# Kernel tuning notes

Hardware: AMD Instinct MI355X
Metric: run time of the kernel (lower is better)

The kernel has to match this reference:

```python
import jax, jax.numpy as jnp
import numpy as np

C, NC, B, T, H, W = 64, 4, 4, 8, 96, 96
BT = B * T
_DN = ('NCDHW', 'OIDHW', 'NCDHW')


def setup_inputs() -> dict:
    key = jax.random.key(0)
    ks = jax.random.split(key, 16)
    r = lambda i, shape, s=0.02: jax.random.normal(ks[i], shape, jnp.float32) * s
    f32 = jnp.float32
    return {
        'x': jax.random.normal(ks[0], (BT, C, H, W), f32),
        't': T,
        'temporal_kernels': r(1, (NC, C)),            # (num_components, C) per-channel kernel scale
        'kernel_weights': jnp.ones((NC,), f32),
        'length_scales': jnp.ones((NC,), f32),
        'temporal_basis': r(2, (C, T)),               # (C, 8) learned temporal basis
        'sc_w1': r(3, (C // 8, C), 0.05), 'sc_b1': jnp.zeros((C // 8,), f32),
        'sc_w2': r(4, (2 * C, C // 8), 0.05), 'sc_b2': jnp.zeros((2 * C,), f32),
        'diff_w': r(5, (C, 1, 3, 1, 1), 0.1),         # depthwise temporal conv
        'diff_gamma': jnp.ones((C,), f32), 'diff_beta': jnp.zeros((C,), f32),
        'diff_mean': r(6, (C,), 0.1),
        'diff_var': jnp.ones((C,), f32) + 0.1 * jax.random.uniform(ks[7], (C,), f32),
        'unc_w1': r(8, (C // 4, C), 0.05), 'unc_b1': jnp.zeros((C // 4,), f32),
        'unc_w2': r(9, (2, C // 4), 0.05), 'unc_b2': jnp.zeros((2,), f32),
        'pool_w': r(10, (C, C, 3, 1, 1), 0.02), 'pool_b': jnp.zeros((C,), f32),
        'proj_w': r(11, (C, C), 0.05),                # spectral-normalized 1x1x1 conv
        'bn_gamma': jnp.ones((C,), f32), 'bn_beta': jnp.zeros((C,), f32),
        'bn_mean': r(12, (C,), 0.1),
        'bn_var': jnp.ones((C,), f32) + 0.1 * jax.random.uniform(ks[13], (C,), f32),
        'temperature': jnp.float32(1.0),
    }


def _bc(v):
    return v[None, :, None, None, None]


def reference(x, t, temporal_kernels, kernel_weights, length_scales, temporal_basis,
              sc_w1, sc_b1, sc_w2, sc_b2,
              diff_w, diff_gamma, diff_beta, diff_mean, diff_var,
              unc_w1, unc_b1, unc_w2, unc_b2,
              pool_w, pool_b, proj_w,
              bn_gamma, bn_beta, bn_mean, bn_var, temperature):
    bt, c, h, w = x.shape
    b = bt // t
    x5 = x.reshape(b, t, c, h, w).transpose(0, 2, 1, 3, 4)   # (b,c,t,h,w)

    # --- Gaussian process temporal attention: per-channel (t,t) RBF mixture kernel ---
    ti = jnp.arange(t, dtype=x.dtype)
    dt2 = (ti[:, None] - ti[None, :]) ** 2                    # (t,t)
    ls = jnp.exp(length_scales)                               # (nc,)
    rbf = jnp.exp(-dt2[None] / (2.0 * ls[:, None, None] ** 2))  # (nc,t,t)
    wts = jax.nn.softmax(kernel_weights)
    K = jnp.einsum('i,ic,ist->cst', wts, temporal_kernels, rbf)  # (c,t,t)
    gp = jnp.einsum('cst,bctn->bcsn', K, x5.reshape(b, c, t, h * w)).reshape(b, c, t, h, w)

    # --- stochastic temporal sampling (eval: deterministic importance mask) ---
    mask = jax.nn.softmax(temporal_basis.mean(axis=0))        # (t,)
    stoch = x5 * mask[None, None, :, None, None]

    # --- spatial covariance gate (global pooled MLP -> sigmoid gate) ---
    g = x5.mean(axis=(2, 3, 4))                               # (b,c)
    h1 = jax.nn.gelu(g @ sc_w1.T + sc_b1, approximate=False)
    cov = h1 @ sc_w2.T + sc_b2                                # (b,2c); second half = cov_var
    cov_w = jax.nn.sigmoid(cov[:, c:])[:, :, None, None, None]
    fused0 = gp * cov_w + stoch * (1.0 - cov_w)

    # --- diffusion: depthwise temporal conv + BN(eval) + GELU ---
    d = jax.lax.conv_general_dilated(fused0, diff_w, (1, 1, 1), ((1, 1), (0, 0), (0, 0)),
                                     dimension_numbers=_DN, feature_group_count=c)
    d = _bc(diff_gamma) * (d - _bc(diff_mean)) / jnp.sqrt(_bc(diff_var) + 1e-5) + _bc(diff_beta)
    d = jax.nn.gelu(d, approximate=False)

    # --- uncertainty head + precision-weighted fusion ---
    u = jax.nn.gelu(jnp.einsum('bcthw,oc->bothw', d, unc_w1) + _bc(unc_b1), approximate=False)
    u = jnp.einsum('bcthw,oc->bothw', u, unc_w2) + _bc(unc_b2)  # (b,2,t,h,w)
    mu, var = u[:, :1], u[:, 1:]
    prec = 1.0 / (var + 1e-6)
    fused = (mu * prec + d) / (prec + 1.0)

    # --- temporal pool: temporal conv then global spatial mean ---
    p = jax.lax.conv_general_dilated(fused, pool_w, (1, 1, 1), ((1, 1), (0, 0), (0, 0)),
                                     dimension_numbers=_DN) + _bc(pool_b)
    out = fused + p.mean(axis=(3, 4), keepdims=True)

    # --- spectral-normalized 1x1x1 projection + BN(eval) ---
    sigma = jnp.linalg.svd(proj_w, compute_uv=False)[0]
    out = jnp.einsum('bcthw,oc->bothw', out, proj_w / sigma)
    out = _bc(bn_gamma) * (out - _bc(bn_mean)) / jnp.sqrt(_bc(bn_var) + 1e-5) + _bc(bn_beta)

    out = out.transpose(0, 2, 1, 3, 4).reshape(bt, c, h, w)
    return x + jnp.tanh(temperature) * out
```

## Files before the change

kernel.cpp:

```cpp
#include <hip/hip_runtime.h>
#include <math.h>

#define C64 64
#define NCK 4
#define BB  4
#define TT  8
#define HH  96
#define WW  96
#define HW  9216
#define CHW (C64*HW)
#define NTILE 32
#define NBLK_PER_B (HW/NTILE)

#define OFF_GSUM 0
#define OFF_S    256
#define OFF_COVW 2304
#define OFF_K    2560
#define OFF_MASK 6656
#define OFF_AC   6664
#define OFF_BC   6728
#define OFF_P2   6792
#define OFF_B2   10888
#define OFF_BIAS3 10952
#define ZERO_N   2304

__device__ __forceinline__ float gelu_f(float v) {
    return 0.5f * v * (1.0f + erff(v * 0.70710678118654752f));
}
__device__ __forceinline__ unsigned short f2bf(float f) {
    union { float f; unsigned int u; } v; v.f = f;
    unsigned int r = (v.u + 0x7fffu + ((v.u >> 16) & 1u)) >> 16;
    return (unsigned short)r;
}
__device__ __forceinline__ float bf2f(unsigned short h) {
    union { unsigned int u; float f; } v; v.u = ((unsigned int)h) << 16;
    return v.f;
}

__global__ __launch_bounds__(256) void k1_gsum(const float* __restrict__ x,
                                               float* __restrict__ ws) {
    const int blk = blockIdx.x;
    const float4* p = reinterpret_cast<const float4*>(x + (size_t)blk * HW);
    float s = 0.f;
    for (int i = threadIdx.x; i < HW / 4; i += 256) {
        float4 v = p[i];
        s += v.x + v.y + v.z + v.w;
    }
    #pragma unroll
    for (int off = 32; off; off >>= 1) s += __shfl_down(s, off, 64);
    __shared__ float part[4];
    const int wid = threadIdx.x >> 6, lane = threadIdx.x & 63;
    if (lane == 0) part[wid] = s;
    __syncthreads();
    if (threadIdx.x == 0) {
        float t = part[0] + part[1] + part[2] + part[3];
        int c = blk % C64;
        int b = (blk / C64) / TT;
        atomicAdd(ws + OFF_GSUM + b * C64 + c, t);
    }
}

__global__ __launch_bounds__(256) void k2_prep(
    const float* __restrict__ tk, const float* __restrict__ kw,
    const float* __restrict__ lsc, const float* __restrict__ tb,
    const float* __restrict__ sc_w1, const float* __restrict__ sc_b1,
    const float* __restrict__ sc_w2, const float* __restrict__ sc_b2,
    const float* __restrict__ diff_gamma, const float* __restrict__ diff_beta,
    const float* __restrict__ diff_mean, const float* __restrict__ diff_var,
    const float* __restrict__ proj_w,
    const float* __restrict__ bn_gamma, const float* __restrict__ bn_beta,
    const float* __restrict__ bn_mean, const float* __restrict__ bn_var,
    const float* __restrict__ temperature,
    float* __restrict__ ws) {
    __shared__ float gsh[BB * C64];
    __shared__ float h1[BB][8];
    __shared__ float wtss[NCK], lss[NCK];
    __shared__ float Msh[64 * 64];
    __shared__ float M2sh[64 * 64];
    __shared__ float v0[64], v1[64];
    __shared__ float lamsh;
    const int tid = threadIdx.x;

    gsh[tid] = ws[OFF_GSUM + tid] * (1.0f / ((float)TT * (float)HW));
    __syncthreads();

    if (tid < BB * 8) {
        int b = tid >> 3, j = tid & 7;
        float a = sc_b1[j];
        for (int c = 0; c < C64; c++) a += gsh[b * C64 + c] * sc_w1[j * C64 + c];
        h1[b][j] = gelu_f(a);
    }
    if (tid == 0) {
        float mx = -1e30f;
        for (int i = 0; i < NCK; i++) mx = fmaxf(mx, kw[i]);
        float e[NCK], s = 0.f;
        for (int i = 0; i < NCK; i++) { e[i] = expf(kw[i] - mx); s += e[i]; }
        for (int i = 0; i < NCK; i++) { wtss[i] = e[i] / s; lss[i] = expf(lsc[i]); }
    }
    if (tid == 1) {
        float m[TT], mx = -1e30f;
        for (int t = 0; t < TT; t++) {
            float a = 0.f;
            for (int c = 0; c < C64; c++) a += tb[c * TT + t];
            m[t] = a * (1.0f / (float)C64);
            mx = fmaxf(mx, m[t]);
        }
        float s = 0.f;
        for (int t = 0; t < TT; t++) { m[t] = expf(m[t] - mx); s += m[t]; }
        for (int t = 0; t < TT; t++) ws[OFF_MASK + t] = m[t] / s;
    }
    __syncthreads();

    {
        int b = tid >> 6, c = tid & 63;
        float a = sc_b2[C64 + c];
        for (int j = 0; j < 8; j++) a += h1[b][j] * sc_w2[(C64 + c) * 8 + j];
        ws[OFF_COVW + b * C64 + c] = 1.f / (1.f + expf(-a));
    }
    for (int q = tid; q < C64 * TT * TT; q += 256) {
        int c = q >> 6, s8 = (q >> 3) & 7, t8 = q & 7;
        float dt = (float)(s8 - t8);
        float dt2 = dt * dt;
        float a = 0.f;
        for (int i = 0; i < NCK; i++)
            a += wtss[i] * tk[i * C64 + c] * expf(-dt2 / (2.f * lss[i] * lss[i]));
        ws[OFF_K + q] = a;
    }
    if (tid < C64) {
        float ac = diff_gamma[tid] * rsqrtf(diff_var[tid] + 1e-5f);
        ws[OFF_AC + tid] = ac;
        ws[OFF_BC + tid] = diff_beta[tid] - ac * diff_mean[tid];
    }
    for (int q = tid; q < 4096; q += 256) {
        int i = q >> 6, j = q & 63;
        float a = 0.f;
        for (int k = 0; k < 64; k++) a += proj_w[k * 64 + i] * proj_w[k * 64 + j];
        Msh[q] = a;
    }
    __syncthreads();
    for (int q = tid; q < 4096; q += 256) {
        int i = q >> 6, j = q & 63;
        float a = 0.f;
        for (int k = 0; k < 64; k++) a += Msh[i * 64 + k] * Msh[k * 64 + j];
        M2sh[q] = a;
    }
    if (tid < 64) v0[tid] = 1.f;
    __syncthreads();
    for (int it = 0; it < 40; ++it) {
        float y = 0.f;
        if (tid < 64) {
            for (int k = 0; k < 64; k++) y += M2sh[k * 64 + tid] * v0[k];
        }
        float yy = y * y;
        #pragma unroll
        for (int off = 32; off; off >>= 1) yy += __shfl_down(yy, off, 64);
        float nrm = __shfl(yy, 0, 64);
        if (tid < 64) v1[tid] = y * rsqrtf(fmaxf(nrm, 1e-30f));
        __syncthreads();
        if (tid < 64) v0[tid] = v1[tid];
        __syncthreads();
    }
    {
        float a = 0.f;
        if (tid < 64) {
            for (int k = 0; k < 64; k++) a += Msh[k * 64 + tid] * v0[k];
            a *= v0[tid];
        }
        #pragma unroll
        for (int off = 32; off; off >>= 1) a += __shfl_down(a, off, 64);
        if (tid == 0) lamsh = a;
    }
    __syncthreads();
    const float sigma = sqrtf(fmaxf(lamsh, 1e-30f));
    const float tau = tanhf(temperature[0]);
    if (tid < 64) {
        float gp = bn_gamma[tid] * rsqrtf(bn_var[tid] + 1e-5f);
        ws[OFF_B2 + tid] = tau * (bn_beta[tid] - gp * bn_mean[tid]);
    }
    for (int q = tid; q < 4096; q += 256) {
        int o = q >> 6, c = q & 63;
        float gp = bn_gamma[o] * rsqrtf(bn_var[o] + 1e-5f);
        ws[OFF_P2 + q] = tau * gp * proj_w[o * 64 + c] / sigma;
    }
}

__device__ __forceinline__ void compute_tile(
    const float* __restrict__ x, const float* __restrict__ diff_w,
    const float* __restrict__ unc_w1, const float* __restrict__ unc_b1,
    const float* __restrict__ unc_w2, const float* __restrict__ unc_b2,
    const float* __restrict__ ws, int b, int n0,
    unsigned short* dls, float* alph, float* bet) {
    const int tid = threadIdx.x;
    const int nloc = tid & 31;
    const int n = n0 + nloc;
    float mk[TT];
    #pragma unroll
    for (int t = 0; t < TT; t++) mk[t] = ws[OFF_MASK + t];

    #pragma unroll
    for (int p = 0; p < 8; p++) {
        const int c = (tid >> 5) + (p << 3);
        float xr[TT];
        #pragma unroll
        for (int t = 0; t < TT; t++)
            xr[t] = x[(size_t)((b * TT + t) * C64 + c) * HW + n];
        const float cw = ws[OFF_COVW + b * C64 + c];
        const float* kr = ws + OFF_K + c * (TT * TT);
        float f0[TT];
        #pragma unroll
        for (int s = 0; s < TT; s++) {
            float a = 0.f;
            #pragma unroll
            for (int t = 0; t < TT; t++) a += kr[s * TT + t] * xr[t];
            f0[s] = a * cw + xr[s] * mk[s] * (1.f - cw);
        }
        const float w0 = diff_w[c * 3 + 0], w1 = diff_w[c * 3 + 1], w2 = diff_w[c * 3 + 2];
        const float ac = ws[OFF_AC + c], bc = ws[OFF_BC + c];
        #pragma unroll
        for (int t = 0; t < TT; t++) {
            float pre = w1 * f0[t];
            if (t > 0)      pre += w0 * f0[t - 1];
            if (t < TT - 1) pre += w2 * f0[t + 1];
            dls[(c * TT + t) * NTILE + nloc] = f2bf(gelu_f(ac * pre + bc));
        }
    }
    __syncthreads();

    {
        const int t = tid >> 5;
        float dcol[C64];
        #pragma unroll
        for (int c = 0; c < C64; c++) dcol[c] = bf2f(dls[(c * TT + t) * NTILE + nloc]);
        float u1[16];
        #pragma unroll
        for (int o = 0; o < 16; o++) {
            float a = unc_b1[o];
            const float* wr = unc_w1 + o * C64;
            #pragma unroll
            for (int c = 0; c < C64; c++) a += wr[c] * dcol[c];
            u1[o] = gelu_f(a);
        }
        float mu = unc_b2[0], va = unc_b2[1];
        #pragma unroll
        for (int o = 0; o < 16; o++) {
            mu += unc_w2[o] * u1[o];
            va += unc_w2[16 + o] * u1[o];
        }
        const float vp = va + 1e-6f;
        const float inv = 1.f / (1.f + vp);
        alph[tid] = vp * inv;
        bet[tid] = mu * inv;
    }
    __syncthreads();
}

__global__ __launch_bounds__(256) void k3_main(
    const float* __restrict__ x, const float* __restrict__ diff_w,
    const float* __restrict__ unc_w1, const float* __restrict__ unc_b1,
    const float* __restrict__ unc_w2, const float* __restrict__ unc_b2,
    float* __restrict__ ws, float* __restrict__ out) {
    __shared__ unsigned short dls[C64 * TT * NTILE];
    __shared__ float alph[256], bet[256];
    const int tile = blockIdx.x;
    const int b = tile / NBLK_PER_B;
    const int n0 = (tile % NBLK_PER_B) * NTILE;
    compute_tile(x, diff_w, unc_w1, unc_b1, unc_w2, unc_b2, ws, b, n0, dls, alph, bet);
    const int tid = threadIdx.x, nloc = tid & 31;

    #pragma unroll
    for (int p = 0; p < 8; p++) {
        const int c = (tid >> 5) + (p << 3);
        #pragma unroll
        for (int t = 0; t < TT; t++) {
            const int idx = (c * TT + t) * NTILE + nloc;
            float f = alph[t * 32 + nloc] * bf2f(dls[idx]) + bet[t * 32 + nloc];
            dls[idx] = f2bf(f);
            float v = f;
            #pragma unroll
            for (int off = 16; off; off >>= 1) v += __shfl_xor(v, off, 32);
            if (nloc == 0) atomicAdd(ws + OFF_S + (b * C64 + c) * TT + t, v);
        }
    }
    __syncthreads();

    {
        const int t = tid >> 5;
        float fcol[C64];
        #pragma unroll
        for (int c = 0; c < C64; c++) fcol[c] = bf2f(dls[(c * TT + t) * NTILE + nloc]);
        const size_t xb = (size_t)(b * TT + t) * CHW + n0 + nloc;
        for (int o = 0; o < C64; o++) {
            const float4* pr4 = reinterpret_cast<const float4*>(ws + OFF_P2 + o * C64);
            float a = 0.f;
            #pragma unroll
            for (int c4 = 0; c4 < 16; c4++) {
                float4 w4 = pr4[c4];
                a += w4.x * fcol[c4 * 4 + 0];
                a += w4.y * fcol[c4 * 4 + 1];
                a += w4.z * fcol[c4 * 4 + 2];
                a += w4.w * fcol[c4 * 4 + 3];
            }
            out[xb + (size_t)o * HW] = x[xb + (size_t)o * HW] + a;
        }
    }
}

__global__ __launch_bounds__(64) void k4_bias(
    const float* __restrict__ pool_w, const float* __restrict__ pool_b,
    float* __restrict__ ws) {
    const int b = blockIdx.x >> 3, t = blockIdx.x & 7;
    const int o = threadIdx.x;
    __shared__ float pm[C64];
    float a = 0.f;
    for (int k = 0; k < 3; k++) {
        int tt = t + k - 1;
        if (tt < 0 || tt >= TT) continue;
        const float* Sp = ws + OFF_S + b * C64 * TT + tt;
        for (int cp = 0; cp < C64; cp++)
            a += pool_w[(o * C64 + cp) * 3 + k] * Sp[cp * TT];
    }
    pm[o] = pool_b[o] + a * (1.0f / (float)HW);
    __syncthreads();
    float bb = ws[OFF_B2 + o];
    const float* pr = ws + OFF_P2 + o * C64;
    for (int c = 0; c < C64; c++) bb += pr[c] * pm[c];
    ws[OFF_BIAS3 + (b * C64 + o) * TT + t] = bb;
}

__global__ __launch_bounds__(256) void k5_bias(
    const float* __restrict__ ws, float* __restrict__ out) {
    const int plane = blockIdx.x;
    const int o = plane & 63;
    const int bt = plane >> 6;
    const int b = bt >> 3, t = bt & 7;
    const float bias = ws[OFF_BIAS3 + (b * C64 + o) * TT + t];
    float4* p = reinterpret_cast<float4*>(out + (size_t)plane * HW);
    #pragma unroll
    for (int i = 0; i < 9; i++) {
        const int idx = threadIdx.x + i * 256;
        float4 v = p[idx];
        v.x += bias; v.y += bias; v.z += bias; v.w += bias;
        p[idx] = v;
    }
}

extern "C" void kernel_launch(void* const* d_in, const int* in_sizes, int n_in,
                              void* d_out, int out_size, void* d_ws, size_t ws_size,
                              hipStream_t stream) {
    const float* x           = (const float*)d_in[0];
    const float* tk          = (const float*)d_in[2];
    const float* kw          = (const float*)d_in[3];
    const float* lsc         = (const float*)d_in[4];
    const float* tb          = (const float*)d_in[5];
    const float* sc_w1       = (const float*)d_in[6];
    const float* sc_b1       = (const float*)d_in[7];
    const float* sc_w2       = (const float*)d_in[8];
    const float* sc_b2       = (const float*)d_in[9];
    const float* diff_w      = (const float*)d_in[10];
    const float* diff_gamma  = (const float*)d_in[11];
    const float* diff_beta   = (const float*)d_in[12];
    const float* diff_mean   = (const float*)d_in[13];
    const float* diff_var    = (const float*)d_in[14];
    const float* unc_w1      = (const float*)d_in[15];
    const float* unc_b1      = (const float*)d_in[16];
    const float* unc_w2      = (const float*)d_in[17];
    const float* unc_b2      = (const float*)d_in[18];
    const float* pool_w      = (const float*)d_in[19];
    const float* pool_b      = (const float*)d_in[20];
    const float* proj_w      = (const float*)d_in[21];
    const float* bn_gamma    = (const float*)d_in[22];
    const float* bn_beta     = (const float*)d_in[23];
    const float* bn_mean     = (const float*)d_in[24];
    const float* bn_var      = (const float*)d_in[25];
    const float* temperature = (const float*)d_in[26];
    float* ws = (float*)d_ws;
    float* out = (float*)d_out;

    hipMemsetAsync(ws, 0, ZERO_N * sizeof(float), stream);
    k1_gsum<<<dim3(BB * TT * C64), dim3(256), 0, stream>>>(x, ws);
    k2_prep<<<dim3(1), dim3(256), 0, stream>>>(tk, kw, lsc, tb, sc_w1, sc_b1,
                                               sc_w2, sc_b2, diff_gamma, diff_beta,
                                               diff_mean, diff_var, proj_w, bn_gamma,
                                               bn_beta, bn_mean, bn_var, temperature, ws);
    k3_main<<<dim3(BB * NBLK_PER_B), dim3(256), 0, stream>>>(x, diff_w, unc_w1, unc_b1,
                                                             unc_w2, unc_b2, ws, out);
    k4_bias<<<dim3(BB * TT), dim3(64), 0, stream>>>(pool_w, pool_b, ws);
    k5_bias<<<dim3(BB * TT * C64), dim3(256), 0, stream>>>(ws, out);
}
```

Before: 601.7 us.

## Use bf16 MFMA for projection GEMM with swizzled row-major LDS tile

```diff
diff --git a/kernel.cpp b/kernel.cpp
--- a/kernel.cpp
+++ b/kernel.cpp
@@ -22,7 +22,11 @@
 #define OFF_P2   6792
 #define OFF_B2   10888
 #define OFF_BIAS3 10952
+#define OFF_P2BF 13000
 #define ZERO_N   2304
+
+typedef __attribute__((ext_vector_type(8))) short short8;
+typedef __attribute__((ext_vector_type(4))) float f32x4;
 
 __device__ __forceinline__ float gelu_f(float v) {
     return 0.5f * v * (1.0f + erff(v * 0.70710678118654752f));
@@ -35,6 +39,9 @@
 __device__ __forceinline__ float bf2f(unsigned short h) {
     union { unsigned int u; float f; } v; v.u = ((unsigned int)h) << 16;
     return v.f;
+}
+__device__ __forceinline__ int swz(int tn, int c) {
+    return (tn << 6) + (c ^ ((tn & 7) << 3));
 }
 
 __global__ __launch_bounds__(256) void k1_gsum(const float* __restrict__ x,
@@ -146,7 +153,7 @@
     }
     if (tid < 64) v0[tid] = 1.f;
     __syncthreads();
-    for (int it = 0; it < 40; ++it) {
+    for (int it = 0; it < 24; ++it) {
         float y = 0.f;
         if (tid < 64) {
             for (int k = 0; k < 64; k++) y += M2sh[k * 64 + tid] * v0[k];
@@ -177,130 +184,154 @@
         float gp = bn_gamma[tid] * rsqrtf(bn_var[tid] + 1e-5f);
         ws[OFF_B2 + tid] = tau * (bn_beta[tid] - gp * bn_mean[tid]);
     }
-    for (int q = tid; q < 4096; q += 256) {
-        int o = q >> 6, c = q & 63;
-        float gp = bn_gamma[o] * rsqrtf(bn_var[o] + 1e-5f);
-        ws[OFF_P2 + q] = tau * gp * proj_w[o * 64 + c] / sigma;
-    }
-}
-
-__device__ __forceinline__ void compute_tile(
-    const float* __restrict__ x, const float* __restrict__ diff_w,
-    const float* __restrict__ unc_w1, const float* __restrict__ unc_b1,
-    const float* __restrict__ unc_w2, const float* __restrict__ unc_b2,
-    const float* __restrict__ ws, int b, int n0,
-    unsigned short* dls, float* alph, float* bet) {
-    const int tid = threadIdx.x;
-    const int nloc = tid & 31;
-    const int n = n0 + nloc;
-    float mk[TT];
-    #pragma unroll
-    for (int t = 0; t < TT; t++) mk[t] = ws[OFF_MASK + t];
-
-    #pragma unroll
-    for (int p = 0; p < 8; p++) {
-        const int c = (tid >> 5) + (p << 3);
-        float xr[TT];
-        #pragma unroll
-        for (int t = 0; t < TT; t++)
-            xr[t] = x[(size_t)((b * TT + t) * C64 + c) * HW + n];
-        const float cw = ws[OFF_COVW + b * C64 + c];
-        const float* kr = ws + OFF_K + c * (TT * TT);
-        float f0[TT];
-        #pragma unroll
-        for (int s = 0; s < TT; s++) {
-            float a = 0.f;
-            #pragma unroll
-            for (int t = 0; t < TT; t++) a += kr[s * TT + t] * xr[t];
-            f0[s] = a * cw + xr[s] * mk[s] * (1.f - cw);
-        }
-        const float w0 = diff_w[c * 3 + 0], w1 = diff_w[c * 3 + 1], w2 = diff_w[c * 3 + 2];
-        const float ac = ws[OFF_AC + c], bc = ws[OFF_BC + c];
-        #pragma unroll
-        for (int t = 0; t < TT; t++) {
-            float pre = w1 * f0[t];
-            if (t > 0)      pre += w0 * f0[t - 1];
-            if (t < TT - 1) pre += w2 * f0[t + 1];
-            dls[(c * TT + t) * NTILE + nloc] = f2bf(gelu_f(ac * pre + bc));
-        }
-    }
-    __syncthreads();
-
-    {
-        const int t = tid >> 5;
-        float dcol[C64];
-        #pragma unroll
-        for (int c = 0; c < C64; c++) dcol[c] = bf2f(dls[(c * TT + t) * NTILE + nloc]);
-        float u1[16];
-        #pragma unroll
-        for (int o = 0; o < 16; o++) {
-            float a = unc_b1[o];
-            const float* wr = unc_w1 + o * C64;
-            #pragma unroll
-            for (int c = 0; c < C64; c++) a += wr[c] * dcol[c];
-            u1[o] = gelu_f(a);
-        }
-        float mu = unc_b2[0], va = unc_b2[1];
-        #pragma unroll
-        for (int o = 0; o < 16; o++) {
-            mu += unc_w2[o] * u1[o];
-            va += unc_w2[16 + o] * u1[o];
-        }
-        const float vp = va + 1e-6f;
-        const float inv = 1.f / (1.f + vp);
-        alph[tid] = vp * inv;
-        bet[tid] = mu * inv;
-    }
-    __syncthreads();
+    {
+        short* p2b = (short*)(ws + OFF_P2BF);
+        for (int q = tid; q < 4096; q += 256) {
+            int o = q >> 6;
+            float gp = bn_gamma[o] * rsqrtf(bn_var[o] + 1e-5f);
+            float v = tau * gp * proj_w[q] / sigma;
+            ws[OFF_P2 + q] = v;
+            p2b[q] = (short)f2bf(v);
+        }
+    }
 }
 
 __global__ __launch_bounds__(256) void k3_main(
     const float* __restrict__ x, const float* __restrict__ diff_w,
     const float* __restrict__ unc_w1, const float* __restrict__ unc_b1,
     const float* __restrict__ unc_w2, const float* __restrict__ unc_b2,
-    float* __restrict__ ws, float* __restrict__ out) {
-    __shared__ unsigned short dls[C64 * TT * NTILE];
-    __shared__ float alph[256], bet[256];
+    const float* __restrict__ ws, float* __restrict__ out) {
+    __shared__ short dls[256 * 64];
     const int tile = blockIdx.x;
     const int b = tile / NBLK_PER_B;
     const int n0 = (tile % NBLK_PER_B) * NTILE;
-    compute_tile(x, diff_w, unc_w1, unc_b1, unc_w2, unc_b2, ws, b, n0, dls, alph, bet);
-    const int tid = threadIdx.x, nloc = tid & 31;
-
-    #pragma unroll
-    for (int p = 0; p < 8; p++) {
-        const int c = (tid >> 5) + (p << 3);
-        #pragma unroll
-        for (int t = 0; t < TT; t++) {
-            const int idx = (c * TT + t) * NTILE + nloc;
-            float f = alph[t * 32 + nloc] * bf2f(dls[idx]) + bet[t * 32 + nloc];
-            dls[idx] = f2bf(f);
-            float v = f;
-            #pragma unroll
-            for (int off = 16; off; off >>= 1) v += __shfl_xor(v, off, 32);
-            if (nloc == 0) atomicAdd(ws + OFF_S + (b * C64 + c) * TT + t, v);
+    const int tid = threadIdx.x;
+    const int nloc = tid & 31;
+
+    {
+        const int n = n0 + nloc;
+        float mk[TT];
+        #pragma unroll
+        for (int t = 0; t < TT; t++) mk[t] = ws[OFF_MASK + t];
+        #pragma unroll
+        for (int p = 0; p < 8; p++) {
+            const int c = (tid >> 5) + (p << 3);
+            float xr[TT];
+            #pragma unroll
+            for (int t = 0; t < TT; t++)
+                xr[t] = x[(size_t)((b * TT + t) * C64 + c) * HW + n];
+            const float cw = ws[OFF_COVW + b * C64 + c];
+            const float* kr = ws + OFF_K + c * (TT * TT);
+            float f0[TT];
+            #pragma unroll
+            for (int s = 0; s < TT; s++) {
+                float a = 0.f;
+                #pragma unroll
+                for (int t = 0; t < TT; t++) a += kr[s * TT + t] * xr[t];
+                f0[s] = a * cw + xr[s] * mk[s] * (1.f - cw);
+            }
+            const float w0 = diff_w[c * 3 + 0], w1 = diff_w[c * 3 + 1], w2 = diff_w[c * 3 + 2];
+            const float ac = ws[OFF_AC + c], bc = ws[OFF_BC + c];
+            #pragma unroll
+            for (int t = 0; t < TT; t++) {
+                float pre = w1 * f0[t];
+                if (t > 0)      pre += w0 * f0[t - 1];
+                if (t < TT - 1) pre += w2 * f0[t + 1];
+                dls[swz(t * 32 + nloc, c)] = (short)f2bf(gelu_f(ac * pre + bc));
+            }
         }
     }
     __syncthreads();
 
     {
         const int t = tid >> 5;
-        float fcol[C64];
-        #pragma unroll
-        for (int c = 0; c < C64; c++) fcol[c] = bf2f(dls[(c * TT + t) * NTILE + nloc]);
-        const size_t xb = (size_t)(b * TT + t) * CHW + n0 + nloc;
-        for (int o = 0; o < C64; o++) {
-            const float4* pr4 = reinterpret_cast<const float4*>(ws + OFF_P2 + o * C64);
-            float a = 0.f;
-            #pragma unroll
-            for (int c4 = 0; c4 < 16; c4++) {
-                float4 w4 = pr4[c4];
-                a += w4.x * fcol[c4 * 4 + 0];
-                a += w4.y * fcol[c4 * 4 + 1];
-                a += w4.z * fcol[c4 * 4 + 2];
-                a += w4.w * fcol[c4 * 4 + 3];
-            }
-            out[xb + (size_t)o * HW] = x[xb + (size_t)o * HW] + a;
+        float dcol[C64];
+        #pragma unroll
+        for (int j = 0; j < 8; j++) {
+            short8 v = *(const short8*)(dls + swz(tid, j * 8));
+            #pragma unroll
+            for (int i = 0; i < 8; i++) dcol[j * 8 + i] = bf2f((unsigned short)v[i]);
+        }
+        float u1[16];
+        #pragma unroll
+        for (int o = 0; o < 16; o++) {
+            float a = unc_b1[o];
+            const float* wr = unc_w1 + o * C64;
+            #pragma unroll
+            for (int c = 0; c < C64; c++) a += wr[c] * dcol[c];
+            u1[o] = gelu_f(a);
+        }
+        float mu = unc_b2[0], va = unc_b2[1];
+        #pragma unroll
+        for (int o = 0; o < 16; o++) {
+            mu += unc_w2[o] * u1[o];
+            va += unc_w2[16 + o] * u1[o];
+        }
+        const float vp = va + 1e-6f;
+        const float inv = 1.f / (1.f + vp);
+        const float alpha = vp * inv;
+        const float beta = mu * inv;
+
+        #pragma unroll
+        for (int j = 0; j < 8; j++) {
+            short8 wv;
+            #pragma unroll
+            for (int i = 0; i < 8; i++) {
+                float f = alpha * dcol[j * 8 + i] + beta;
+                wv[i] = (short)f2bf(f);
+                float v = f;
+                v += __shfl_xor(v, 1);
+                v += __shfl_xor(v, 2);
+                v += __shfl_xor(v, 4);
+                v += __shfl_xor(v, 8);
+                v += __shfl_xor(v, 16);
+                if ((tid & 31) == 0)
+                    atomicAdd((float*)ws + OFF_S + (b * C64 + (j * 8 + i)) * TT + t, v);
+            }
+            *(short8*)(dls + swz(tid, j * 8)) = wv;
+        }
+    }
+    __syncthreads();
+
+    {
+        const int w = tid >> 6;
+        const int l = tid & 63;
+        const int l15 = l & 15;
+        const int lg = (l >> 4) & 3;
+        const short* P2B = (const short*)(ws + OFF_P2BF);
+        f32x4 acc[4][4] = {};
+        #pragma unroll
+        for (int kh = 0; kh < 2; ++kh) {
+            const int cb = kh * 32 + lg * 8;
+            short8 bfr[4];
+            #pragma unroll
+            for (int nt = 0; nt < 4; ++nt) {
+                const int tn = w * 64 + nt * 16 + l15;
+                bfr[nt] = *(const short8*)(dls + swz(tn, cb));
+            }
+            #pragma unroll
+            for (int mt = 0; mt < 4; ++mt) {
+                const int o = mt * 16 + l15;
+                short8 afr = *(const short8*)(P2B + o * 64 + cb);
+                #pragma unroll
+                for (int nt = 0; nt < 4; ++nt)
+                    acc[mt][nt] = __builtin_amdgcn_mfma_f32_16x16x32_bf16(
+                        afr, bfr[nt], acc[mt][nt], 0, 0, 0);
+            }
+        }
+        #pragma unroll
+        for (int nt = 0; nt < 4; ++nt) {
+            const int t = 2 * w + (nt >> 1);
+            const int nl = (nt & 1) * 16 + l15;
+            #pragma unroll
+            for (int mt = 0; mt < 4; ++mt) {
+                #pragma unroll
+                for (int j = 0; j < 4; ++j) {
+                    const int o = mt * 16 + lg * 4 + j;
+                    const size_t idx = (size_t)((b * TT + t) * C64 + o) * HW + n0 + nl;
+                    out[idx] = x[idx] + acc[mt][nt][j];
+                }
+            }
         }
     }
 }
```

New measurement: 507.8 us. -15.6%, faster.
